# Performance work log

Hardware: AMD Instinct MI355X
Metric: run time of the kernel (lower is better)

Reference implementation:

```python
import jax, jax.numpy as jnp
import numpy as np

DIM = 768
HEADS = 12
HEAD_DIM = 64
INNER = HEADS * HEAD_DIM  # 768


def setup_inputs() -> dict:
    key = jax.random.key(0)
    k_x, k_wqkv, k_bqkv, k_wout, k_bout = jax.random.split(key, 5)
    B, S = 2, 2048
    x = jax.random.normal(k_x, (B, S, DIM), dtype=jnp.float32)
    # nn.Linear(dim, 3*inner): weight [out, in]; store transposed for x @ W
    lim = 1.0 / np.sqrt(DIM)
    w_qkv = jax.random.uniform(k_wqkv, (DIM, 3 * INNER), minval=-lim, maxval=lim, dtype=jnp.float32)
    b_qkv = jax.random.uniform(k_bqkv, (3 * INNER,), minval=-lim, maxval=lim, dtype=jnp.float32)
    lim2 = 1.0 / np.sqrt(INNER)
    # original zero-inits to_out; use random weights so the reference output is non-trivial
    w_out = jax.random.uniform(k_wout, (INNER, DIM), minval=-lim2, maxval=lim2, dtype=jnp.float32)
    b_out = jax.random.uniform(k_bout, (DIM,), minval=-lim2, maxval=lim2, dtype=jnp.float32)
    return {"x": x, "w_qkv": w_qkv, "b_qkv": b_qkv, "w_out": w_out, "b_out": b_out}


def reference(x, w_qkv, b_qkv, w_out, b_out):
    B, S, _ = x.shape
    qkv = x @ w_qkv + b_qkv                               # [B, S, 3*H*D]
    qkv = qkv.reshape(B, S, 3, HEADS, HEAD_DIM)           # b s three h d
    q, k, v = qkv[:, :, 0], qkv[:, :, 1], qkv[:, :, 2]    # each [B, S, H, D]
    scale = 1.0 / np.sqrt(HEAD_DIM)
    # non-causal self-attention (FlashSelfAttention, dropout=0, causal=False)
    scores = jnp.einsum('bshd,bthd->bhst', q, k) * scale  # [B, H, S, S]
    attn = jax.nn.softmax(scores, axis=-1)
    ctx = jnp.einsum('bhst,bthd->bshd', attn, v)          # [B, S, H, D]
    ctx = ctx.reshape(B, S, INNER)
    return ctx @ w_out + b_out                            # [B, S, DIM]
```

## Files before the change

kernel.cpp:

```cpp
#include <hip/hip_runtime.h>
#include <cstddef>
#include <cstdint>

#define DIM  768
#define NH   12
#define HD   64
#define SEQ  2048
#define NB   2
#define NQKV 2304
#define G    (NB * NH * SEQ)

typedef _Float16 f16x8 __attribute__((ext_vector_type(8)));
typedef _Float16 f16x4 __attribute__((ext_vector_type(4)));
typedef __fp16   h16x2 __attribute__((ext_vector_type(2)));
typedef float    f32x4 __attribute__((ext_vector_type(4)));
typedef float    f32x16 __attribute__((ext_vector_type(16)));

#if __has_builtin(__builtin_amdgcn_exp2f)
#define EXP2(x) __builtin_amdgcn_exp2f(x)
#else
#define EXP2(x) exp2f(x)
#endif

#define QSCALE 0.1803368801111244f

__device__ __forceinline__ void gld16(const _Float16* g, _Float16* l) {
  __builtin_amdgcn_global_load_lds(
      (const __attribute__((address_space(1))) void*)g,
      (__attribute__((address_space(3))) void*)l, 16, 0, 0);
}

__device__ __forceinline__ int pkrtz_i(float a, float b) {
  union { h16x2 h; int w; } u;
  u.h = __builtin_amdgcn_cvt_pkrtz(a, b);
  return u.w;
}

__global__ __launch_bounds__(256) void transpose_cvt_kernel(
    const float* __restrict__ W, _Float16* __restrict__ WT, int K, int N) {
  __shared__ _Float16 tl[32][36];
  const int t = threadIdx.x;
  const int k0 = blockIdx.y * 32, n0 = blockIdx.x * 32;
  {
    const int r = t >> 3, c4 = (t & 7) * 4;
    float4 f = *(const float4*)(W + (size_t)(k0 + r) * N + n0 + c4);
    tl[r][c4 + 0] = (_Float16)f.x; tl[r][c4 + 1] = (_Float16)f.y;
    tl[r][c4 + 2] = (_Float16)f.z; tl[r][c4 + 3] = (_Float16)f.w;
  }
  __syncthreads();
  const int n = t >> 3, kc = (t & 7) * 4;
  f16x4 v;
  v[0] = tl[kc + 0][n]; v[1] = tl[kc + 1][n];
  v[2] = tl[kc + 2][n]; v[3] = tl[kc + 3][n];
  *(f16x4*)(WT + (size_t)(n0 + n) * K + k0 + kc) = v;
}

__global__ __launch_bounds__(256) void vtrans_kernel(
    const _Float16* __restrict__ v, _Float16* __restrict__ vT) {
  __shared__ _Float16 tl[64][68];
  const int t = threadIdx.x;
  const int bh = blockIdx.x, st = blockIdx.y;
  const size_t base = (size_t)bh * SEQ * HD;
  {
    const int s = t >> 2, dc = (t & 3) * 16;
    const _Float16* p = v + base + (size_t)(st * 64 + s) * HD + dc;
    f16x8 a = *(const f16x8*)p, b = *(const f16x8*)(p + 8);
    *(f16x8*)&tl[s][dc] = a;
    *(f16x8*)&tl[s][dc + 8] = b;
  }
  __syncthreads();
  const int d = t >> 2, sc = (t & 3) * 16;
  f16x8 o0, o1;
#pragma unroll
  for (int j = 0; j < 8; j++) { o0[j] = tl[sc + j][d]; o1[j] = tl[sc + 8 + j][d]; }
  _Float16* q = vT + base + (size_t)d * SEQ + st * 64 + sc;
  *(f16x8*)q = o0;
  *(f16x8*)(q + 8) = o1;
}

__global__ __launch_bounds__(256) void qkv_gemm_kernel(
    const float* __restrict__ X, const _Float16* __restrict__ BT,
    const float* __restrict__ bias, _Float16* __restrict__ q,
    _Float16* __restrict__ k, _Float16* __restrict__ v) {
  __shared__ _Float16 As[128 * 32];
  __shared__ _Float16 Bs[128 * 32];
  const int tid = threadIdx.x;
  const int lane = tid & 63, wv = tid >> 6;
  const int wm = wv >> 1, wn = wv & 1;
  const int quad = lane >> 4, lcol = lane & 15;
  const int bm = blockIdx.y * 128, bn = blockIdx.x * 128;
  const int K = DIM, N = NQKV;

  f32x4 acc[4][4];
#pragma unroll
  for (int i = 0; i < 4; i++)
#pragma unroll
    for (int j = 0; j < 4; j++) acc[i][j] = (f32x4)(0.f);

  const float* asrc[2];
  _Float16* adst[2];
#pragma unroll
  for (int i = 0; i < 2; i++) {
    const int rA = 64 * i + (tid >> 2);
    const int cc = tid & 3;
    asrc[i] = X + (size_t)(bm + rA) * K + cc * 8;
    adst[i] = As + rA * 32 + ((cc ^ ((rA >> 1) & 3)) * 8);
  }
  const int r0 = wv * 32 + (lane >> 2);
  const int kp = (((lane & 3) ^ ((r0 >> 1) & 3)) * 8);
  const _Float16* b0p = BT + (size_t)(bn + r0) * K + kp;
  const _Float16* b1p = BT + (size_t)(bn + r0 + 16) * K + kp;
  _Float16* lB0 = Bs + (wv * 2 + 0) * 512;
  _Float16* lB1 = Bs + (wv * 2 + 1) * 512;

  for (int k0 = 0; k0 < K; k0 += 32) {
    float4 a0[2], a1[2];
#pragma unroll
    for (int i = 0; i < 2; i++) {
      a0[i] = *(const float4*)(asrc[i] + k0);
      a1[i] = *(const float4*)(asrc[i] + k0 + 4);
    }
    __syncthreads();
    gld16(b0p + k0, lB0);
    gld16(b1p + k0, lB1);
#pragma unroll
    for (int i = 0; i < 2; i++) {
      f16x8 h;
      h[0] = (_Float16)a0[i].x; h[1] = (_Float16)a0[i].y;
      h[2] = (_Float16)a0[i].z; h[3] = (_Float16)a0[i].w;
      h[4] = (_Float16)a1[i].x; h[5] = (_Float16)a1[i].y;
      h[6] = (_Float16)a1[i].z; h[7] = (_Float16)a1[i].w;
      *(f16x8*)adst[i] = h;
    }
    __syncthreads();

    f16x8 af[4], bf[4];
#pragma unroll
    for (int mi = 0; mi < 4; mi++) {
      const int R = wm * 64 + mi * 16 + lcol;
      af[mi] = *(const f16x8*)&As[R * 32 + ((quad ^ ((R >> 1) & 3)) * 8)];
    }
#pragma unroll
    for (int ni = 0; ni < 4; ni++) {
      const int R = wn * 64 + ni * 16 + lcol;
      bf[ni] = *(const f16x8*)&Bs[R * 32 + ((quad ^ ((R >> 1) & 3)) * 8)];
    }
#pragma unroll
    for (int mi = 0; mi < 4; mi++)
#pragma unroll
      for (int ni = 0; ni < 4; ni++)
        acc[mi][ni] = __builtin_amdgcn_mfma_f32_16x16x32_f16(af[mi], bf[ni], acc[mi][ni], 0, 0, 0);
  }

#pragma unroll
  for (int mi = 0; mi < 4; mi++) {
#pragma unroll
    for (int r = 0; r < 4; r++) {
      const int row = bm + wm * 64 + mi * 16 + quad * 4 + r;
      const int b_ = row >> 11, s_ = row & 2047;
#pragma unroll
      for (int ni = 0; ni < 4; ni++) {
        const int c = bn + wn * 64 + ni * 16 + lcol;
        const float val = acc[mi][ni][r] + bias[c];
        const int d = c & 63;
        const int which = c / 768;
        const int h = (c - which * 768) >> 6;
        const size_t idx = (((size_t)b_ * NH + h) * SEQ + s_) * HD + d;
        if (which == 0)      q[idx] = (_Float16)(val * QSCALE);
        else if (which == 1) k[idx] = (_Float16)val;
        else                 v[idx] = (_Float16)val;
      }
    }
  }
}

#define PST 68
#define TILES ((SEQ / 2) / 64)
__global__ __launch_bounds__(256, 3) void attn_part_kernel(
    const _Float16* __restrict__ Q, const _Float16* __restrict__ K,
    const _Float16* __restrict__ V, _Float16* __restrict__ Ohat,
    float* __restrict__ L) {
  __shared__ _Float16 Ks[2][64 * PST];
  __shared__ _Float16 Vs[2][64 * PST];
  __shared__ float lsh[4][32];
  const int tid = threadIdx.x, lane = tid & 63, wv = tid >> 6;
  const int lr = lane & 31, hw = lane >> 5;
  const int bh = blockIdx.x, qt = blockIdx.y, ks = blockIdx.z;
  const size_t base = (size_t)bh * SEQ * HD;

  f16x8 qb[4];
  {
    const _Float16* qp = Q + base + (size_t)(qt * 128 + wv * 32 + lr) * HD + hw * 8;
#pragma unroll
    for (int f = 0; f < 4; f++) qb[f] = *(const f16x8*)(qp + f * 16);
  }

  f32x16 o0 = (f32x16)(0.f), o1 = (f32x16)(0.f);
  float lpa = 0.f, lpb = 0.f;

  const int sr = tid >> 2;
  const int sc = (tid & 3) * 16;
  const _Float16* kp = K + base + (size_t)ks * (SEQ / 2) * HD + (size_t)sr * HD + sc;
  const _Float16* vp = V + base + ks * (SEQ / 2) + (size_t)sr * SEQ + sc;

  f16x8 kr0 = *(const f16x8*)kp, kr1 = *(const f16x8*)(kp + 8);
  f16x8 vr0 = *(const f16x8*)vp, vr1 = *(const f16x8*)(vp + 8);
  *(f16x8*)&Ks[0][sr * PST + sc]     = kr0;
  *(f16x8*)&Ks[0][sr * PST + sc + 8] = kr1;
  *(f16x8*)&Vs[0][sr * PST + sc]     = vr0;
  *(f16x8*)&Vs[0][sr * PST + sc + 8] = vr1;
  kr0 = *(const f16x8*)(kp + 64 * HD); kr1 = *(const f16x8*)(kp + 64 * HD + 8);
  vr0 = *(const f16x8*)(vp + 64);      vr1 = *(const f16x8*)(vp + 64 + 8);
  asm volatile("s_waitcnt lgkmcnt(0)" ::: "memory");

  for (int t = 0; t < TILES; t++) {
    const int cur = t & 1;
    __builtin_amdgcn_s_barrier();
    __builtin_amdgcn_sched_barrier(0);

    f32x16 s0 = (f32x16)(0.f), s1 = (f32x16)(0.f);
    __builtin_amdgcn_s_setprio(1);
#pragma unroll
    for (int f = 0; f < 4; f++) {
      f16x8 ka0 = *(const f16x8*)&Ks[cur][lr * PST + f * 16 + hw * 8];
      f16x8 ka1 = *(const f16x8*)&Ks[cur][(32 + lr) * PST + f * 16 + hw * 8];
      s0 = __builtin_amdgcn_mfma_f32_32x32x16_f16(ka0, qb[f], s0, 0, 0, 0);
      s1 = __builtin_amdgcn_mfma_f32_32x32x16_f16(ka1, qb[f], s1, 0, 0, 0);
    }
    __builtin_amdgcn_s_setprio(0);

    f16x8 pf[4];
#pragma unroll
    for (int f = 0; f < 4; f++) {
      const f32x16& sv = (f < 2) ? s0 : s1;
      const int r0 = (f & 1) * 8;
      const float e0 = EXP2(sv[r0 + 0]), e1 = EXP2(sv[r0 + 1]);
      const float e2 = EXP2(sv[r0 + 2]), e3 = EXP2(sv[r0 + 3]);
      const float e4 = EXP2(sv[r0 + 4]), e5 = EXP2(sv[r0 + 5]);
      const float e6 = EXP2(sv[r0 + 6]), e7 = EXP2(sv[r0 + 7]);
      lpa += (e0 + e1) + (e2 + e3);
      lpb += (e4 + e5) + (e6 + e7);
      const int a01 = pkrtz_i(e0, e1), b45 = pkrtz_i(e4, e5);
      const int c23 = pkrtz_i(e2, e3), d67 = pkrtz_i(e6, e7);
      auto w02 = __builtin_amdgcn_permlane32_swap(a01, b45, false, false);
      auto w13 = __builtin_amdgcn_permlane32_swap(c23, d67, false, false);
      union { f16x8 h; int w[4]; } pu;
      pu.w[0] = w02[0]; pu.w[1] = w13[0]; pu.w[2] = w02[1]; pu.w[3] = w13[1];
      pf[f] = pu.h;
    }

    __builtin_amdgcn_s_setprio(1);
#pragma unroll
    for (int f = 0; f < 4; f++) {
      f16x8 vb0 = *(const f16x8*)&Vs[cur][lr * PST + f * 16 + hw * 8];
      f16x8 vb1 = *(const f16x8*)&Vs[cur][(32 + lr) * PST + f * 16 + hw * 8];
      o0 = __builtin_amdgcn_mfma_f32_32x32x16_f16(pf[f], vb0, o0, 0, 0, 0);
      o1 = __builtin_amdgcn_mfma_f32_32x32x16_f16(pf[f], vb1, o1, 0, 0, 0);
    }
    __builtin_amdgcn_s_setprio(0);

    if (t + 1 < TILES) {
      const int nxt = cur ^ 1;
      *(f16x8*)&Ks[nxt][sr * PST + sc]     = kr0;
      *(f16x8*)&Ks[nxt][sr * PST + sc + 8] = kr1;
      *(f16x8*)&Vs[nxt][sr * PST + sc]     = vr0;
      *(f16x8*)&Vs[nxt][sr * PST + sc + 8] = vr1;
      if (t + 2 < TILES) {
        const _Float16* kn = kp + (size_t)(t + 2) * 64 * HD;
        const _Float16* vn = vp + (t + 2) * 64;
        kr0 = *(const f16x8*)kn; kr1 = *(const f16x8*)(kn + 8);
        vr0 = *(const f16x8*)vn; vr1 = *(const f16x8*)(vn + 8);
      }
      asm volatile("s_waitcnt lgkmcnt(0)" ::: "memory");
    }
  }

  const float l_part = lpa + lpb;
  const float l_full = l_part + __shfl_xor(l_part, 32);
  __syncthreads();
  if (hw == 0) lsh[wv][lr] = l_full;
  __syncthreads();

  const size_t rbase = (size_t)ks * G + (size_t)bh * SEQ + qt * 128 + wv * 32;
  if (hw == 0) L[rbase + lr] = l_full;
  float linv[16];
#pragma unroll
  for (int r = 0; r < 16; r++)
    linv[r] = 1.00048828125f / lsh[wv][(r & 3) + 8 * (r >> 2) + 4 * hw];
#pragma unroll
  for (int r = 0; r < 16; r++) {
    const int rr = (r & 3) + 8 * (r >> 2) + 4 * hw;
    _Float16* cp = Ohat + (rbase + rr) * HD;
    cp[lr]      = (_Float16)(o0[r] * linv[r]);
    cp[32 + lr] = (_Float16)(o1[r] * linv[r]);
  }
}

__global__ __launch_bounds__(256) void out_gemm_kernel(
    const _Float16* __restrict__ Ohat, const float* __restrict__ L,
    const _Float16* __restrict__ WT, const float* __restrict__ bias,
    float* __restrict__ out) {
  __shared__ _Float16 As[64 * 36];
  __shared__ _Float16 Bs[64 * 36];
  const int tid = threadIdx.x, lane = tid & 63, wv = tid >> 6;
  const int wr = (wv >> 1) * 32, wc = (wv & 1) * 32;
  const int quad = lane >> 4, lcol = lane & 15;
  const int bm = blockIdx.y * 64, bn = blockIdx.x * 64;

  f32x4 acc[2][2];
#pragma unroll
  for (int i = 0; i < 2; i++)
#pragma unroll
    for (int j = 0; j < 2; j++) acc[i][j] = (f32x4)(0.f);

  const int ra = tid >> 2, ca = (tid & 3) * 8;
  const int grow = bm + ra, b_ = grow >> 11, s_ = grow & 2047;

  for (int k0 = 0; k0 < DIM; k0 += 32) {
    const int h = k0 >> 6;
    const int lidx = (b_ * NH + h) * SEQ + s_;
    const size_t obase = (size_t)lidx * HD + (k0 & 32) + ca;
    f16x8 u0 = *(const f16x8*)(Ohat + obase);
    f16x8 u1 = *(const f16x8*)(Ohat + (size_t)G * HD + obase);
    const float l0 = L[lidx], l1 = L[G + lidx];
    const float w0 = l0 / (l0 + l1), w1 = 1.0f - w0;
    f16x8 bv = *(const f16x8*)(WT + (size_t)(bn + ra) * DIM + k0 + ca);

    __syncthreads();
    f16x8 av;
#pragma unroll
    for (int j = 0; j < 8; j++)
      av[j] = (_Float16)(w0 * (float)u0[j] + w1 * (float)u1[j]);
    *(f16x8*)&As[ra * 36 + ca] = av;
    *(f16x8*)&Bs[ra * 36 + ca] = bv;
    __syncthreads();

    f16x8 af[2], bf[2];
#pragma unroll
    for (int mi = 0; mi < 2; mi++)
      af[mi] = *(const f16x8*)&As[(wr + mi * 16 + lcol) * 36 + quad * 8];
#pragma unroll
    for (int ni = 0; ni < 2; ni++)
      bf[ni] = *(const f16x8*)&Bs[(wc + ni * 16 + lcol) * 36 + quad * 8];
#pragma unroll
    for (int mi = 0; mi < 2; mi++)
#pragma unroll
      for (int ni = 0; ni < 2; ni++)
        acc[mi][ni] = __builtin_amdgcn_mfma_f32_16x16x32_f16(af[mi], bf[ni], acc[mi][ni], 0, 0, 0);
  }

#pragma unroll
  for (int mi = 0; mi < 2; mi++) {
#pragma unroll
    for (int r = 0; r < 4; r++) {
      const int row = bm + wr + mi * 16 + quad * 4 + r;
#pragma unroll
      for (int ni = 0; ni < 2; ni++) {
        const int col = bn + wc + ni * 16 + lcol;
        out[(size_t)row * DIM + col] = acc[mi][ni][r] + bias[col];
      }
    }
  }
}

extern "C" void kernel_launch(void* const* d_in, const int* in_sizes, int n_in,
                              void* d_out, int out_size, void* d_ws,
                              size_t ws_size, hipStream_t stream) {
  const float* x = (const float*)d_in[0];
  const float* w_qkv = (const float*)d_in[1];
  const float* b_qkv = (const float*)d_in[2];
  const float* w_out = (const float*)d_in[3];
  const float* b_out = (const float*)d_in[4];
  float* out = (float*)d_out;

  _Float16* wsh = (_Float16*)d_ws;
  size_t off = 0;
  const size_t hsz = (size_t)NB * NH * SEQ * HD;
  _Float16* wqkvT = wsh + off; off += (size_t)NQKV * DIM;
  _Float16* woutT = wsh + off; off += (size_t)DIM * DIM;
  _Float16* qh   = wsh + off; off += hsz;
  _Float16* kh   = wsh + off; off += hsz;
  _Float16* vh   = wsh + off; off += hsz;
  _Float16* vT   = wsh + off; off += hsz;
  _Float16* Ohat = wsh + off; off += 2 * hsz;
  float*    Lbuf = (float*)(wsh + off);

  transpose_cvt_kernel<<<dim3(NQKV / 32, DIM / 32), 256, 0, stream>>>(w_qkv, wqkvT, DIM, NQKV);
  transpose_cvt_kernel<<<dim3(DIM / 32, DIM / 32), 256, 0, stream>>>(w_out, woutT, DIM, DIM);
  qkv_gemm_kernel<<<dim3(NQKV / 128, (NB * SEQ) / 128), 256, 0, stream>>>(
      x, wqkvT, b_qkv, qh, kh, vh);
  vtrans_kernel<<<dim3(NB * NH, SEQ / 64), 256, 0, stream>>>(vh, vT);
  attn_part_kernel<<<dim3(NB * NH, SEQ / 128, 2), 256, 0, stream>>>(
      qh, kh, vT, Ohat, Lbuf);
  out_gemm_kernel<<<dim3(DIM / 64, (NB * SEQ) / 64), 256, 0, stream>>>(
      Ohat, Lbuf, woutT, b_out, out);
}
```

Baseline: 172.7 us.

## Double query rows per wave and split keys four ways in attention

Each wave now handles 64 query rows (two 32-row halves) against the same K/V tile, so every LDS K/V fragment load feeds twice as many MFMAs. The key dimension is split into four partitions instead of two, which keeps the grid size constant, and the output GEMM merges four partial results weighted by their softmax sums. In exchange, register pressure rises (occupancy hint lowered to 2), the partial output buffer doubles, and the output GEMM reads twice as many partial rows.

```diff
diff --git a/kernel.cpp b/kernel.cpp
--- a/kernel.cpp
+++ b/kernel.cpp
@@ -175,33 +175,38 @@
 }
 
 #define PST 68
-#define TILES ((SEQ / 2) / 64)
-__global__ __launch_bounds__(256, 3) void attn_part_kernel(
+#define KSPLIT 4
+#define KEYS (SEQ / KSPLIT)
+#define TILES (KEYS / 64)
+__global__ __launch_bounds__(256, 2) void attn_part_kernel(
     const _Float16* __restrict__ Q, const _Float16* __restrict__ K,
     const _Float16* __restrict__ V, _Float16* __restrict__ Ohat,
     float* __restrict__ L) {
   __shared__ _Float16 Ks[2][64 * PST];
   __shared__ _Float16 Vs[2][64 * PST];
-  __shared__ float lsh[4][32];
+  __shared__ float lsh[4][2][32];
   const int tid = threadIdx.x, lane = tid & 63, wv = tid >> 6;
   const int lr = lane & 31, hw = lane >> 5;
   const int bh = blockIdx.x, qt = blockIdx.y, ks = blockIdx.z;
   const size_t base = (size_t)bh * SEQ * HD;
 
-  f16x8 qb[4];
-  {
-    const _Float16* qp = Q + base + (size_t)(qt * 128 + wv * 32 + lr) * HD + hw * 8;
-#pragma unroll
-    for (int f = 0; f < 4; f++) qb[f] = *(const f16x8*)(qp + f * 16);
-  }
-
-  f32x16 o0 = (f32x16)(0.f), o1 = (f32x16)(0.f);
-  float lpa = 0.f, lpb = 0.f;
+  f16x8 qb[2][4];
+#pragma unroll
+  for (int qh = 0; qh < 2; qh++) {
+    const _Float16* qp =
+        Q + base + (size_t)(qt * 256 + wv * 64 + qh * 32 + lr) * HD + hw * 8;
+#pragma unroll
+    for (int f = 0; f < 4; f++) qb[qh][f] = *(const f16x8*)(qp + f * 16);
+  }
+
+  f32x16 o00 = (f32x16)(0.f), o01 = (f32x16)(0.f);
+  f32x16 o10 = (f32x16)(0.f), o11 = (f32x16)(0.f);
+  float lpa0 = 0.f, lpb0 = 0.f, lpa1 = 0.f, lpb1 = 0.f;
 
   const int sr = tid >> 2;
   const int sc = (tid & 3) * 16;
-  const _Float16* kp = K + base + (size_t)ks * (SEQ / 2) * HD + (size_t)sr * HD + sc;
-  const _Float16* vp = V + base + ks * (SEQ / 2) + (size_t)sr * SEQ + sc;
+  const _Float16* kp = K + base + (size_t)ks * KEYS * HD + (size_t)sr * HD + sc;
+  const _Float16* vp = V + base + ks * KEYS + (size_t)sr * SEQ + sc;
 
   f16x8 kr0 = *(const f16x8*)kp, kr1 = *(const f16x8*)(kp + 8);
   f16x8 vr0 = *(const f16x8*)vp, vr1 = *(const f16x8*)(vp + 8);
@@ -218,35 +223,61 @@
     __builtin_amdgcn_s_barrier();
     __builtin_amdgcn_sched_barrier(0);
 
-    f32x16 s0 = (f32x16)(0.f), s1 = (f32x16)(0.f);
+    f16x8 ka0[4], ka1[4];
+#pragma unroll
+    for (int f = 0; f < 4; f++) {
+      ka0[f] = *(const f16x8*)&Ks[cur][lr * PST + f * 16 + hw * 8];
+      ka1[f] = *(const f16x8*)&Ks[cur][(32 + lr) * PST + f * 16 + hw * 8];
+    }
+
+    f32x16 s00 = (f32x16)(0.f), s01 = (f32x16)(0.f);
+    f32x16 s10 = (f32x16)(0.f), s11 = (f32x16)(0.f);
     __builtin_amdgcn_s_setprio(1);
 #pragma unroll
     for (int f = 0; f < 4; f++) {
-      f16x8 ka0 = *(const f16x8*)&Ks[cur][lr * PST + f * 16 + hw * 8];
-      f16x8 ka1 = *(const f16x8*)&Ks[cur][(32 + lr) * PST + f * 16 + hw * 8];
-      s0 = __builtin_amdgcn_mfma_f32_32x32x16_f16(ka0, qb[f], s0, 0, 0, 0);
-      s1 = __builtin_amdgcn_mfma_f32_32x32x16_f16(ka1, qb[f], s1, 0, 0, 0);
+      s00 = __builtin_amdgcn_mfma_f32_32x32x16_f16(ka0[f], qb[0][f], s00, 0, 0, 0);
+      s01 = __builtin_amdgcn_mfma_f32_32x32x16_f16(ka1[f], qb[0][f], s01, 0, 0, 0);
+      s10 = __builtin_amdgcn_mfma_f32_32x32x16_f16(ka0[f], qb[1][f], s10, 0, 0, 0);
+      s11 = __builtin_amdgcn_mfma_f32_32x32x16_f16(ka1[f], qb[1][f], s11, 0, 0, 0);
     }
     __builtin_amdgcn_s_setprio(0);
 
-    f16x8 pf[4];
+    f16x8 pf0[4], pf1[4];
 #pragma unroll
     for (int f = 0; f < 4; f++) {
-      const f32x16& sv = (f < 2) ? s0 : s1;
+      const f32x16& sv = (f < 2) ? s00 : s01;
       const int r0 = (f & 1) * 8;
       const float e0 = EXP2(sv[r0 + 0]), e1 = EXP2(sv[r0 + 1]);
       const float e2 = EXP2(sv[r0 + 2]), e3 = EXP2(sv[r0 + 3]);
       const float e4 = EXP2(sv[r0 + 4]), e5 = EXP2(sv[r0 + 5]);
       const float e6 = EXP2(sv[r0 + 6]), e7 = EXP2(sv[r0 + 7]);
-      lpa += (e0 + e1) + (e2 + e3);
-      lpb += (e4 + e5) + (e6 + e7);
+      lpa0 += (e0 + e1) + (e2 + e3);
+      lpb0 += (e4 + e5) + (e6 + e7);
       const int a01 = pkrtz_i(e0, e1), b45 = pkrtz_i(e4, e5);
       const int c23 = pkrtz_i(e2, e3), d67 = pkrtz_i(e6, e7);
       auto w02 = __builtin_amdgcn_permlane32_swap(a01, b45, false, false);
       auto w13 = __builtin_amdgcn_permlane32_swap(c23, d67, false, false);
       union { f16x8 h; int w[4]; } pu;
       pu.w[0] = w02[0]; pu.w[1] = w13[0]; pu.w[2] = w02[1]; pu.w[3] = w13[1];
-      pf[f] = pu.h;
+      pf0[f] = pu.h;
+    }
+#pragma unroll
+    for (int f = 0; f < 4; f++) {
+      const f32x16& sv = (f < 2) ? s10 : s11;
+      const int r0 = (f & 1) * 8;
+      const float e0 = EXP2(sv[r0 + 0]), e1 = EXP2(sv[r0 + 1]);
+      const float e2 = EXP2(sv[r0 + 2]), e3 = EXP2(sv[r0 + 3]);
+      const float e4 = EXP2(sv[r0 + 4]), e5 = EXP2(sv[r0 + 5]);
+      const float e6 = EXP2(sv[r0 + 6]), e7 = EXP2(sv[r0 + 7]);
+      lpa1 += (e0 + e1) + (e2 + e3);
+      lpb1 += (e4 + e5) + (e6 + e7);
+      const int a01 = pkrtz_i(e0, e1), b45 = pkrtz_i(e4, e5);
+      const int c23 = pkrtz_i(e2, e3), d67 = pkrtz_i(e6, e7);
+      auto w02 = __builtin_amdgcn_permlane32_swap(a01, b45, false, false);
+      auto w13 = __builtin_amdgcn_permlane32_swap(c23, d67, false, false);
+      union { f16x8 h; int w[4]; } pu;
+      pu.w[0] = w02[0]; pu.w[1] = w13[0]; pu.w[2] = w02[1]; pu.w[3] = w13[1];
+      pf1[f] = pu.h;
     }
 
     __builtin_amdgcn_s_setprio(1);
@@ -254,8 +285,10 @@
     for (int f = 0; f < 4; f++) {
       f16x8 vb0 = *(const f16x8*)&Vs[cur][lr * PST + f * 16 + hw * 8];
       f16x8 vb1 = *(const f16x8*)&Vs[cur][(32 + lr) * PST + f * 16 + hw * 8];
-      o0 = __builtin_amdgcn_mfma_f32_32x32x16_f16(pf[f], vb0, o0, 0, 0, 0);
-      o1 = __builtin_amdgcn_mfma_f32_32x32x16_f16(pf[f], vb1, o1, 0, 0, 0);
+      o00 = __builtin_amdgcn_mfma_f32_32x32x16_f16(pf0[f], vb0, o00, 0, 0, 0);
+      o01 = __builtin_amdgcn_mfma_f32_32x32x16_f16(pf0[f], vb1, o01, 0, 0, 0);
+      o10 = __builtin_amdgcn_mfma_f32_32x32x16_f16(pf1[f], vb0, o10, 0, 0, 0);
+      o11 = __builtin_amdgcn_mfma_f32_32x32x16_f16(pf1[f], vb1, o11, 0, 0, 0);
     }
     __builtin_amdgcn_s_setprio(0);
 
@@ -275,24 +308,30 @@
     }
   }
 
-  const float l_part = lpa + lpb;
-  const float l_full = l_part + __shfl_xor(l_part, 32);
+  float l0 = lpa0 + lpb0; l0 += __shfl_xor(l0, 32);
+  float l1 = lpa1 + lpb1; l1 += __shfl_xor(l1, 32);
   __syncthreads();
-  if (hw == 0) lsh[wv][lr] = l_full;
+  if (hw == 0) { lsh[wv][0][lr] = l0; lsh[wv][1][lr] = l1; }
   __syncthreads();
 
-  const size_t rbase = (size_t)ks * G + (size_t)bh * SEQ + qt * 128 + wv * 32;
-  if (hw == 0) L[rbase + lr] = l_full;
-  float linv[16];
-#pragma unroll
-  for (int r = 0; r < 16; r++)
-    linv[r] = 1.00048828125f / lsh[wv][(r & 3) + 8 * (r >> 2) + 4 * hw];
-#pragma unroll
-  for (int r = 0; r < 16; r++) {
-    const int rr = (r & 3) + 8 * (r >> 2) + 4 * hw;
-    _Float16* cp = Ohat + (rbase + rr) * HD;
-    cp[lr]      = (_Float16)(o0[r] * linv[r]);
-    cp[32 + lr] = (_Float16)(o1[r] * linv[r]);
+#pragma unroll
+  for (int qh = 0; qh < 2; qh++) {
+    const f32x16& oa = qh ? o10 : o00;
+    const f32x16& ob = qh ? o11 : o01;
+    const size_t rbase =
+        (size_t)ks * G + (size_t)bh * SEQ + qt * 256 + wv * 64 + qh * 32;
+    if (hw == 0) L[rbase + lr] = qh ? l1 : l0;
+    float linv[16];
+#pragma unroll
+    for (int r = 0; r < 16; r++)
+      linv[r] = 1.00048828125f / lsh[wv][qh][(r & 3) + 8 * (r >> 2) + 4 * hw];
+#pragma unroll
+    for (int r = 0; r < 16; r++) {
+      const int rr = (r & 3) + 8 * (r >> 2) + 4 * hw;
+      _Float16* cp = Ohat + (rbase + rr) * HD;
+      cp[lr]      = (_Float16)(oa[r] * linv[r]);
+      cp[32 + lr] = (_Float16)(ob[r] * linv[r]);
+    }
   }
 }
 
@@ -322,15 +361,20 @@
     const size_t obase = (size_t)lidx * HD + (k0 & 32) + ca;
     f16x8 u0 = *(const f16x8*)(Ohat + obase);
     f16x8 u1 = *(const f16x8*)(Ohat + (size_t)G * HD + obase);
+    f16x8 u2 = *(const f16x8*)(Ohat + 2 * (size_t)G * HD + obase);
+    f16x8 u3 = *(const f16x8*)(Ohat + 3 * (size_t)G * HD + obase);
     const float l0 = L[lidx], l1 = L[G + lidx];
-    const float w0 = l0 / (l0 + l1), w1 = 1.0f - w0;
+    const float l2 = L[2 * G + lidx], l3 = L[3 * G + lidx];
+    const float inv = 1.0f / ((l0 + l1) + (l2 + l3));
+    const float w0 = l0 * inv, w1 = l1 * inv, w2 = l2 * inv, w3 = l3 * inv;
     f16x8 bv = *(const f16x8*)(WT + (size_t)(bn + ra) * DIM + k0 + ca);
 
     __syncthreads();
     f16x8 av;
 #pragma unroll
     for (int j = 0; j < 8; j++)
-      av[j] = (_Float16)(w0 * (float)u0[j] + w1 * (float)u1[j]);
+      av[j] = (_Float16)((w0 * (float)u0[j] + w1 * (float)u1[j]) +
+                         (w2 * (float)u2[j] + w3 * (float)u3[j]));
     *(f16x8*)&As[ra * 36 + ca] = av;
     *(f16x8*)&Bs[ra * 36 + ca] = bv;
     __syncthreads();
@@ -382,7 +426,7 @@
   _Float16* kh   = wsh + off; off += hsz;
   _Float16* vh   = wsh + off; off += hsz;
   _Float16* vT   = wsh + off; off += hsz;
-  _Float16* Ohat = wsh + off; off += 2 * hsz;
+  _Float16* Ohat = wsh + off; off += 4 * hsz;
   float*    Lbuf = (float*)(wsh + off);
 
   transpose_cvt_kernel<<<dim3(NQKV / 32, DIM / 32), 256, 0, stream>>>(w_qkv, wqkvT, DIM, NQKV);
@@ -390,7 +434,7 @@
   qkv_gemm_kernel<<<dim3(NQKV / 128, (NB * SEQ) / 128), 256, 0, stream>>>(
       x, wqkvT, b_qkv, qh, kh, vh);
   vtrans_kernel<<<dim3(NB * NH, SEQ / 64), 256, 0, stream>>>(vh, vT);
-  attn_part_kernel<<<dim3(NB * NH, SEQ / 128, 2), 256, 0, stream>>>(
+  attn_part_kernel<<<dim3(NB * NH, SEQ / 256, KSPLIT), 256, 0, stream>>>(
       qh, kh, vT, Ohat, Lbuf);
   out_gemm_kernel<<<dim3(DIM / 64, (NB * SEQ) / 64), 256, 0, stream>>>(
       Ohat, Lbuf, woutT, b_out, out);
```

After: 182.2 us. 1.05x slower.
